# Optimization experiments

Hardware: AMD Instinct MI355X
Metric: run time of the kernel (lower is better)

The kernel has to match this reference:

```python
import jax, jax.numpy as jnp
import numpy as np

BS, NPTS, NQ, N, E = 8, 4096, 4096, 1024, 8192
F_, D, DY, H, OUT, STEPS = 256, 2, 3, 256, 3, 16


def setup_inputs() -> dict:
    key = jax.random.key(0)
    ks = jax.random.split(key, 12)
    s = 0.05
    return {
        "inp_x": jax.random.uniform(ks[0], (BS, NPTS, D), dtype=jnp.float32),
        "inp_y": jax.random.normal(ks[1], (BS, NPTS, DY), dtype=jnp.float32),
        "q": jax.random.uniform(ks[2], (BS, NQ, D), dtype=jnp.float32),
        "node_pos": jax.random.uniform(ks[3], (N, D), dtype=jnp.float32),
        "W_e1": jax.random.normal(ks[4], (D + DY, H), dtype=jnp.float32) * s,
        "b_e1": jnp.zeros((H,), jnp.float32),
        "W_e2": jax.random.normal(ks[5], (H, F_), dtype=jnp.float32) * s,
        "b_e2": jnp.zeros((F_,), jnp.float32),
        "W_g": jax.random.normal(ks[6], (F_ + D, F_), dtype=jnp.float32) * s,
        "b_g": jnp.zeros((F_,), jnp.float32),
        "ln_g": jnp.ones((F_,), jnp.float32),
        "ln_b": jnp.zeros((F_,), jnp.float32),
        "W_d1": jax.random.normal(ks[7], (F_ + D, H), dtype=jnp.float32) * s,
        "b_d1": jnp.zeros((H,), jnp.float32),
        "W_d2": jax.random.normal(ks[8], (H, OUT), dtype=jnp.float32) * s,
        "b_d2": jnp.zeros((OUT,), jnp.float32),
        "edge_index": jax.random.randint(ks[9], (2, E), 0, N, dtype=jnp.int32),
        "msg_steps": STEPS,
    }


def _mlp(x, W1, b1, W2, b2):
    # 2-layer ReLU MLP (matches repo's NN encoder/decoder structure)
    return jnp.maximum(x @ W1 + b1, 0.0) @ W2 + b2


def _soft_coord(pos, x):
    # GENSoftNN repr_fn: softmax over nodes of -||x - pos||^2.
    # pos [N,D], x [B,P,D] -> [B,P,N]; expand ||x-p||^2 to avoid [B,P,N,D].
    d = (jnp.sum(x * x, -1)[..., None]
         + jnp.sum(pos * pos, -1)[None, None, :]
         - 2.0 * jnp.einsum('bpd,nd->bpn', x, pos))
    return jax.nn.softmax(-d, axis=-1)


def _layer_norm(x, g, b, eps=1e-5):
    m = jnp.mean(x, -1, keepdims=True)
    v = jnp.mean((x - m) ** 2, -1, keepdims=True)  # biased var, torch LN
    return (x - m) * jax.lax.rsqrt(v + eps) * g + b


def reference(inp_x, inp_y, q, node_pos, W_e1, b_e1, W_e2, b_e2, W_g, b_g,
              ln_g, ln_b, W_d1, b_d1, W_d2, b_d2, edge_index, msg_steps):
    n = node_pos.shape[0]
    # --- GCNConv symmetric normalization with self-loops (PyG default) ---
    loops = jnp.arange(n, dtype=edge_index.dtype)
    src = jnp.concatenate([edge_index[0], loops])  # message source (x_j)
    dst = jnp.concatenate([edge_index[1], loops])  # aggregation target
    deg = jnp.zeros((n,), jnp.float32).at[dst].add(1.0)
    dinv = jax.lax.rsqrt(jnp.maximum(deg, 1e-12))
    norm = (dinv[src] * dinv[dst])[None, :, None]  # [1, E+N, 1]

    # --- encode input points and project onto nodes ---
    enc = _mlp(jnp.concatenate([inp_x, inp_y], -1), W_e1, b_e1, W_e2, b_e2)  # [B,P,F]
    inp_coord = _soft_coord(node_pos, inp_x)                                  # [B,P,N]
    x = jnp.einsum('bpn,bpf->bnf', inp_coord, enc)                            # [B,N,F]

    pos_b = jnp.broadcast_to(node_pos[None], (x.shape[0], n, node_pos.shape[1]))

    # --- msg_steps of  LN(x + GCNConv(cat(pos, x))) ---
    def step(x, _):
        h = jnp.concatenate([pos_b, x], -1) @ W_g        # lin first: [B,N,F]
        msg = h[:, src, :] * norm                         # gather + scale
        agg = jnp.zeros_like(h).at[:, dst, :].add(msg) + b_g  # scatter-add
        return _layer_norm(x + agg, ln_g, ln_b), None

    x, _ = jax.lax.scan(step, x, None, length=msg_steps)

    # --- decode queries ---
    q_coord = _soft_coord(node_pos, q)                    # [B,Q,N]
    lat = jnp.einsum('bqn,bnf->bqf', q_coord, x)          # [B,Q,F]
    return _mlp(jnp.concatenate([lat, q], -1), W_d1, b_d1, W_d2, b_d2)
```

## Files before the change

kernel.cpp:

```cpp
#include <hip/hip_runtime.h>

#define BB 8
#define NP 4096
#define NN 1024
#define NE 8192
#define FF 256
#define TS 264
#define NSTEP 16
#define NSEG 64
#define SEGSZ 128

typedef float f32x4_t __attribute__((ext_vector_type(4)));
typedef __bf16 bf16x8_t __attribute__((ext_vector_type(8)));
typedef unsigned int u32x4_t __attribute__((ext_vector_type(4)));
typedef unsigned int u32x2_t __attribute__((ext_vector_type(2)));

static __device__ __forceinline__ unsigned short f2bf(float f) {
  return __builtin_bit_cast(unsigned short, static_cast<__bf16>(f));
}
static __device__ __forceinline__ float ashf(unsigned short s) {
  union { unsigned u; float f; } t; t.u = (unsigned)s << 16; return t.f;
}
static __device__ __forceinline__ void split_pk(float a, float b, unsigned& h, unsigned& l) {
  unsigned short ha = f2bf(a), hb = f2bf(b);
  unsigned short la = f2bf(a - ashf(ha)), lb = f2bf(b - ashf(hb));
  h = (unsigned)ha | ((unsigned)hb << 16);
  l = (unsigned)la | ((unsigned)lb << 16);
}
static __device__ __forceinline__ f32x4_t mfma16(u32x4_t a, u32x4_t b, f32x4_t c) {
  return __builtin_amdgcn_mfma_f32_16x16x32_bf16(
      __builtin_bit_cast(bf16x8_t, a), __builtin_bit_cast(bf16x8_t, b), c, 0, 0, 0);
}
static __device__ __forceinline__ int swz16(int e) { return e ^ ((e >> 3) & 7); }

__global__ __launch_bounds__(1024) void k_cnt(const int* __restrict__ dstA,
                                              int* __restrict__ cntg) {
  __shared__ int ds[SEGSZ];
  int seg = blockIdx.x, n = threadIdx.x;
  if (n < SEGSZ) ds[n] = dstA[seg * SEGSZ + n];
  __syncthreads();
  int c = 0;
  #pragma unroll 8
  for (int e = 0; e < SEGSZ; e++) c += (ds[e] == n) ? 1 : 0;
  cntg[seg * NN + n] = c;
}

__global__ __launch_bounds__(1024) void k_scan2(const int* __restrict__ cntg,
    float* __restrict__ dinv, int* __restrict__ csr_off) {
  __shared__ int s[NN];
  int n = threadIdx.x;
  int c = 1;
  for (int sg = 0; sg < NSEG; sg++) c += cntg[sg * NN + n];
  dinv[n] = rsqrtf((float)c);
  s[n] = c;
  __syncthreads();
  for (int st = 1; st < NN; st <<= 1) {
    int v = (n >= st) ? s[n - st] : 0;
    __syncthreads();
    s[n] += v;
    __syncthreads();
  }
  csr_off[n] = s[n] - c;
  if (n == NN - 1) csr_off[NN] = s[n];
}

__global__ __launch_bounds__(1024) void k_fill2(const int* __restrict__ srcA,
    const int* __restrict__ dstA, const float* __restrict__ dinv,
    const int* __restrict__ csr_off, const int* __restrict__ cntg,
    int* __restrict__ csr_src, float* __restrict__ csr_w) {
  int n = threadIdx.x;
  if (blockIdx.x == NSEG) {
    int pos = csr_off[n + 1] - 1;
    csr_src[pos] = n;
    csr_w[pos] = dinv[n] * dinv[n];
    return;
  }
  __shared__ int ds[SEGSZ], ss[SEGSZ];
  int seg = blockIdx.x;
  if (n < SEGSZ) { ds[n] = dstA[seg * SEGSZ + n]; ss[n] = srcA[seg * SEGSZ + n]; }
  __syncthreads();
  int base = csr_off[n];
  for (int s2 = 0; s2 < seg; s2++) base += cntg[s2 * NN + n];
  float dn = dinv[n];
  for (int e = 0; e < SEGSZ; e++) {
    if (ds[e] == n) {
      int sv = ss[e];
      csr_src[base] = sv;
      csr_w[base] = dinv[sv] * dn;
      base++;
    }
  }
}

__global__ __launch_bounds__(256) void k_spos(const float* __restrict__ npos,
    const int* __restrict__ csr_off, const int* __restrict__ csr_src,
    const float* __restrict__ csr_w, float* __restrict__ spos) {
  int n = blockIdx.x * 256 + threadIdx.x;
  if (n >= NN) return;
  float sx = 0.f, sy = 0.f;
  int e1 = csr_off[n + 1];
  for (int e = csr_off[n]; e < e1; e++) {
    float w = csr_w[e]; int s = csr_src[e];
    sx += w * npos[2 * s]; sy += w * npos[2 * s + 1];
  }
  spos[2 * n] = sx; spos[2 * n + 1] = sy;
}

__global__ __launch_bounds__(256) void k_posb(const float* __restrict__ spos,
    const float* __restrict__ Wg, const float* __restrict__ bg, float* __restrict__ sposW) {
  int n = blockIdx.x, f = threadIdx.x;
  sposW[(size_t)n * FF + f] = spos[2 * n] * Wg[f] + spos[2 * n + 1] * Wg[FF + f] + bg[f];
}

__global__ __launch_bounds__(256) void k_stats(const float* __restrict__ inx,
    const float* __restrict__ qxy, const float* __restrict__ npos,
    float* __restrict__ mI, float* __restrict__ liI,
    float* __restrict__ mQ, float* __restrict__ liQ) {
  const float* xy = blockIdx.y ? qxy : inx;
  float* mOut = blockIdx.y ? mQ : mI;
  float* liOut = blockIdx.y ? liQ : liI;
  int wv = threadIdx.x >> 6, lane = threadIdx.x & 63;
  int pt = blockIdx.x * 4 + wv;
  float px = xy[pt * 2], py = xy[pt * 2 + 1];
  float s[16];
  float m = -1e30f;
  #pragma unroll
  for (int k = 0; k < 16; k++) {
    int n = lane + 64 * k;
    float2 np = ((const float2*)npos)[n];
    float dx = px - np.x, dy = py - np.y;
    float v = -(dx * dx + dy * dy);
    s[k] = v; m = fmaxf(m, v);
  }
  #pragma unroll
  for (int o = 32; o; o >>= 1) m = fmaxf(m, __shfl_xor(m, o));
  float l = 0.f;
  #pragma unroll
  for (int k = 0; k < 16; k++) l += __expf(s[k] - m);
  #pragma unroll
  for (int o = 32; o; o >>= 1) l += __shfl_xor(l, o);
  if (lane == 0) { mOut[pt] = m; liOut[pt] = 1.0f / l; }
}

__global__ __launch_bounds__(256) void k_pack_w(const float* __restrict__ We2,
    const float* __restrict__ Wg, const float* __restrict__ Wd1,
    unsigned short* __restrict__ WTe2h, unsigned short* __restrict__ WTe2l,
    unsigned short* __restrict__ WTgh, unsigned short* __restrict__ WTgl,
    unsigned short* __restrict__ WTd1h, unsigned short* __restrict__ WTd1l) {
  int kc = blockIdx.x, which = blockIdx.y, n = threadIdx.x;
  const float* W = (which == 0) ? We2 : (which == 1) ? (Wg + 2 * FF) : Wd1;
  unsigned short* Dh = (which == 0) ? WTe2h : (which == 1) ? WTgh : WTd1h;
  unsigned short* Dl = (which == 0) ? WTe2l : (which == 1) ? WTgl : WTd1l;
  unsigned hu[16], lu[16];
  #pragma unroll
  for (int i = 0; i < 16; i++) {
    float a = W[(kc * 32 + 2 * i) * FF + n];
    float b = W[(kc * 32 + 2 * i + 1) * FF + n];
    split_pk(a, b, hu[i], lu[i]);
  }
  u32x4_t* dvh = (u32x4_t*)(Dh + ((size_t)kc * 256 + n) * 32);
  u32x4_t* dvl = (u32x4_t*)(Dl + ((size_t)kc * 256 + n) * 32);
  #pragma unroll
  for (int i = 0; i < 4; i++) {
    u32x4_t th = {hu[4 * i], hu[4 * i + 1], hu[4 * i + 2], hu[4 * i + 3]};
    u32x4_t tl = {lu[4 * i], lu[4 * i + 1], lu[4 * i + 2], lu[4 * i + 3]};
    dvh[i] = th; dvl[i] = tl;
  }
}

__global__ __launch_bounds__(256) void k_encoder(const float* __restrict__ inx,
    const float* __restrict__ iny, const float* __restrict__ We1,
    const float* __restrict__ be1, const unsigned short* __restrict__ WTe2h,
    const unsigned short* __restrict__ WTe2l, const float* __restrict__ be2,
    unsigned short* __restrict__ encTh, unsigned short* __restrict__ encTl) {
  __shared__ float xin[32][8];
  __shared__ float h[32][TS];
  __shared__ unsigned short Bh[8192];
  __shared__ unsigned short Bl[8192];
  int tid = threadIdx.x;
  int row0 = blockIdx.x * 32;
  int wv = tid >> 6, L = tid & 63, lhi = L >> 4, llo = L & 15;

  if (tid < 160) {
    int pt = tid / 5, d = tid % 5;
    int r = row0 + pt;
    xin[pt][d] = (d < 2) ? inx[r * 2 + d] : iny[r * 3 + (d - 2)];
  }
  __syncthreads();
  {
    int f = tid;
    float w0 = We1[f], w1 = We1[256 + f], w2 = We1[512 + f], w3 = We1[768 + f], w4 = We1[1024 + f];
    float bb = be1[f];
    #pragma unroll 4
    for (int pt = 0; pt < 32; pt++) {
      float v = bb + xin[pt][0]*w0 + xin[pt][1]*w1 + xin[pt][2]*w2 + xin[pt][3]*w3 + xin[pt][4]*w4;
      h[pt][f] = fmaxf(v, 0.f);
    }
  }

  f32x4_t acc[2][4];
  #pragma unroll
  for (int cb = 0; cb < 4; cb++) {
    float bc = be2[wv * 64 + cb * 16 + llo];
    f32x4_t t = {bc, bc, bc, bc};
    acc[0][cb] = t; acc[1][cb] = t;
  }

  for (int kc = 0; kc < 8; kc++) {
    __syncthreads();
    {
      const u32x4_t* sh = (const u32x4_t*)(WTe2h + (size_t)kc * 8192);
      const u32x4_t* sl = (const u32x4_t*)(WTe2l + (size_t)kc * 8192);
      u32x4_t* dh = (u32x4_t*)Bh;
      u32x4_t* dl = (u32x4_t*)Bl;
      #pragma unroll
      for (int i = 0; i < 4; i++) {
        int e = tid + i * 256;
        int es = swz16(e);
        dh[es] = sh[e]; dl[es] = sl[e];
      }
    }
    __syncthreads();
    int kbase = kc * 32 + lhi * 8;
    u32x4_t a0h, a0l, a1h, a1l;
    {
      float p[8];
      *(f32x4_t*)p = *(const f32x4_t*)&h[llo][kbase];
      *(f32x4_t*)(p + 4) = *(const f32x4_t*)&h[llo][kbase + 4];
      unsigned hw[4], lw[4];
      #pragma unroll
      for (int i = 0; i < 4; i++) split_pk(p[2 * i], p[2 * i + 1], hw[i], lw[i]);
      u32x4_t th = {hw[0], hw[1], hw[2], hw[3]}; a0h = th;
      u32x4_t tl = {lw[0], lw[1], lw[2], lw[3]}; a0l = tl;
    }
    {
      float p[8];
      *(f32x4_t*)p = *(const f32x4_t*)&h[llo + 16][kbase];
      *(f32x4_t*)(p + 4) = *(const f32x4_t*)&h[llo + 16][kbase + 4];
      unsigned hw[4], lw[4];
      #pragma unroll
      for (int i = 0; i < 4; i++) split_pk(p[2 * i], p[2 * i + 1], hw[i], lw[i]);
      u32x4_t th = {hw[0], hw[1], hw[2], hw[3]}; a1h = th;
      u32x4_t tl = {lw[0], lw[1], lw[2], lw[3]}; a1l = tl;
    }
    #pragma unroll
    for (int cb = 0; cb < 4; cb++) {
      int col = wv * 64 + cb * 16 + llo;
      int off = swz16(col * 4 + lhi) * 8;
      u32x4_t bh = *(const u32x4_t*)&Bh[off];
      u32x4_t bl = *(const u32x4_t*)&Bl[off];
      acc[0][cb] = mfma16(a0h, bh, mfma16(a0h, bl, mfma16(a0l, bh, acc[0][cb])));
      acc[1][cb] = mfma16(a1h, bh, mfma16(a1h, bl, mfma16(a1l, bh, acc[1][cb])));
    }
  }
  #pragma unroll
  for (int rb = 0; rb < 2; rb++)
    #pragma unroll
    for (int cb = 0; cb < 4; cb++) {
      int col = wv * 64 + cb * 16 + llo;
      f32x4_t v = acc[rb][cb];
      size_t idx = ((size_t)blockIdx.x * 256 + col) * 32 + rb * 16 + lhi * 4;
      unsigned hw0, lw0, hw1, lw1;
      split_pk(v[0], v[1], hw0, lw0);
      split_pk(v[2], v[3], hw1, lw1);
      u32x2_t wh = {hw0, hw1}; *(u32x2_t*)&encTh[idx] = wh;
      u32x2_t wl = {lw0, lw1}; *(u32x2_t*)&encTl[idx] = wl;
    }
}

__global__ __launch_bounds__(256, 4) void k_proj1(const float* __restrict__ inx,
    const float* __restrict__ mI, const float* __restrict__ liI,
    const float* __restrict__ npos, const unsigned short* __restrict__ encTh,
    const unsigned short* __restrict__ encTl, float* __restrict__ part) {
  __shared__ unsigned short BstH[8192];
  __shared__ unsigned short BstL[8192];
  __shared__ unsigned short AstH[1024];
  __shared__ unsigned short AstL[1024];
  int tid = threadIdx.x;
  int id = blockIdx.x;
  int xcd = id & 7, kid = id >> 3;
  int slice = xcd * 4 + (kid >> 5);
  int n0 = (kid & 31) * 32;
  int b = slice >> 2, z = slice & 3;
  int wv = tid >> 6, L = tid & 63, lhi = L >> 4, llo = L & 15;
  int an = tid >> 3, t7 = tid & 7, ap = t7 * 4;
  float2 npv = ((const float2*)npos)[n0 + an];
  int pbase0 = b * NP + z * 1024;
  int aoff = swz16(an * 4 + (t7 >> 1)) * 8 + (t7 & 1) * 4;

  u32x4_t rbh[4], rbl[4];
  unsigned ch0, ch1, cl0, cl1;

  auto coordA = [&](int kc) {
    int p = pbase0 + kc * 32 + ap;
    float c[4];
    #pragma unroll
    for (int j = 0; j < 4; j++) {
      float2 pxy = ((const float2*)inx)[p + j];
      float mm = mI[p + j], ll = liI[p + j];
      float dx = pxy.x - npv.x, dy = pxy.y - npv.y;
      c[j] = __expf(-(dx * dx + dy * dy) - mm) * ll;
    }
    split_pk(c[0], c[1], ch0, cl0);
    split_pk(c[2], c[3], ch1, cl1);
  };
  auto loadB = [&](int kc) {
    const u32x4_t* sh = (const u32x4_t*)(encTh + (size_t)(b * 128 + z * 32 + kc) * 8192);
    const u32x4_t* sl = (const u32x4_t*)(encTl + (size_t)(b * 128 + z * 32 + kc) * 8192);
    #pragma unroll
    for (int i = 0; i < 4; i++) { rbh[i] = sh[tid + i * 256]; rbl[i] = sl[tid + i * 256]; }
  };

  f32x4_t acc[2][4];
  #pragma unroll
  for (int i = 0; i < 2; i++)
    #pragma unroll
    for (int j = 0; j < 4; j++) { f32x4_t t = {0.f, 0.f, 0.f, 0.f}; acc[i][j] = t; }

  coordA(0);
  loadB(0);
  int a0off = swz16(llo * 4 + lhi) * 8;
  int a1off = swz16((llo + 16) * 4 + lhi) * 8;
  for (int kc = 0; kc < 32; kc++) {
    __syncthreads();
    #pragma unroll
    for (int i = 0; i < 4; i++) {
      int es = swz16(tid + i * 256);
      ((u32x4_t*)BstH)[es] = rbh[i];
      ((u32x4_t*)BstL)[es] = rbl[i];
    }
    { u32x2_t wh = {ch0, ch1}; *(u32x2_t*)&AstH[aoff] = wh; }
    { u32x2_t wl = {cl0, cl1}; *(u32x2_t*)&AstL[aoff] = wl; }
    __syncthreads();
    if (kc < 31) { loadB(kc + 1); coordA(kc + 1); }
    u32x4_t a0h = *(const u32x4_t*)&AstH[a0off];
    u32x4_t a0l = *(const u32x4_t*)&AstL[a0off];
    u32x4_t a1h = *(const u32x4_t*)&AstH[a1off];
    u32x4_t a1l = *(const u32x4_t*)&AstL[a1off];
    #pragma unroll
    for (int cb = 0; cb < 4; cb++) {
      int off = swz16((wv * 64 + cb * 16 + llo) * 4 + lhi) * 8;
      u32x4_t bh = *(const u32x4_t*)&BstH[off];
      u32x4_t bl = *(const u32x4_t*)&BstL[off];
      acc[0][cb] = mfma16(a0h, bh, mfma16(a0h, bl, mfma16(a0l, bh, acc[0][cb])));
      acc[1][cb] = mfma16(a1h, bh, mfma16(a1h, bl, mfma16(a1l, bh, acc[1][cb])));
    }
  }
  float* op = part + (((size_t)(z * BB + b)) * NN + n0) * FF;
  #pragma unroll
  for (int rb = 0; rb < 2; rb++)
    #pragma unroll
    for (int cb = 0; cb < 4; cb++) {
      int col = wv * 64 + cb * 16 + llo;
      f32x4_t v = acc[rb][cb];
      #pragma unroll
      for (int r = 0; r < 4; r++) op[(rb * 16 + lhi * 4 + r) * FF + col] = v[r];
    }
}

__global__ __launch_bounds__(256) void k_reduce(const float* __restrict__ part,
                                                float* __restrict__ x) {
  size_t i = ((size_t)blockIdx.x * 256 + threadIdx.x) * 4;
  const size_t S = (size_t)BB * NN * FF;
  f32x4_t a = *(const f32x4_t*)&part[i];
  f32x4_t b = *(const f32x4_t*)&part[S + i];
  f32x4_t c = *(const f32x4_t*)&part[2 * S + i];
  f32x4_t d = *(const f32x4_t*)&part[3 * S + i];
  f32x4_t r = (a + b) + (c + d);
  *(f32x4_t*)&x[i] = r;
}

__global__ __launch_bounds__(512) void k_msg2(const float* __restrict__ x_in,
    float* __restrict__ x_out, const float* __restrict__ sposW,
    const int* __restrict__ coff, const int* __restrict__ csrc,
    const float* __restrict__ csw, const unsigned short* __restrict__ WTgh,
    const unsigned short* __restrict__ WTgl, const float* __restrict__ lng,
    const float* __restrict__ lnb, int last,
    unsigned short* __restrict__ xTh, unsigned short* __restrict__ xTl) {
  __shared__ unsigned Ah[32][132];
  __shared__ unsigned Al[32][132];
  __shared__ unsigned short Bh[2][8192];
  __shared__ unsigned short Bl[2][8192];
  __shared__ float redS[32][8];
  __shared__ float redQ[32][8];
  int tid = threadIdx.x;
  int id = blockIdx.x;
  int b = id & 7;
  int nb = id >> 3;
  int n0 = nb * 32;
  int wv = tid >> 6, L = tid & 63, lhi = L >> 4, llo = L & 15;

  u32x4_t rbh[2], rbl[2];
  auto loadB = [&](int kc) {
    const u32x4_t* sh = (const u32x4_t*)(WTgh + (size_t)kc * 8192);
    const u32x4_t* sl = (const u32x4_t*)(WTgl + (size_t)kc * 8192);
    #pragma unroll
    for (int i = 0; i < 2; i++) { rbh[i] = sh[tid + i * 512]; rbl[i] = sl[tid + i * 512]; }
  };
  auto writeB = [&](int buf) {
    u32x4_t* dh = (u32x4_t*)Bh[buf];
    u32x4_t* dl = (u32x4_t*)Bl[buf];
    #pragma unroll
    for (int i = 0; i < 2; i++) {
      int es = swz16(tid + i * 512);
      dh[es] = rbh[i]; dl[es] = rbl[i];
    }
  };

  loadB(0);

  {
    int row = tid >> 4, seg = tid & 15;
    int n = n0 + row;
    float g[16];
    #pragma unroll
    for (int i = 0; i < 16; i++) g[i] = 0.f;
    int e0 = coff[n], e1 = coff[n + 1];
    for (int e = e0; e < e1; e++) {
      float w = csw[e];
      int s = csrc[e];
      const f32x4_t* px = (const f32x4_t*)(x_in + ((size_t)b * NN + s) * FF + seg * 16);
      #pragma unroll
      for (int i = 0; i < 4; i++) {
        f32x4_t v = px[i];
        g[4*i]   += w * v[0]; g[4*i+1] += w * v[1];
        g[4*i+2] += w * v[2]; g[4*i+3] += w * v[3];
      }
    }
    #pragma unroll
    for (int i = 0; i < 8; i++) {
      unsigned h, l;
      split_pk(g[2 * i], g[2 * i + 1], h, l);
      Ah[row][seg * 8 + i] = h;
      Al[row][seg * 8 + i] = l;
    }
  }
  writeB(0);
  __syncthreads();

  f32x4_t acc[2][2];
  #pragma unroll
  for (int i = 0; i < 2; i++)
    #pragma unroll
    for (int j = 0; j < 2; j++) { f32x4_t t = {0.f, 0.f, 0.f, 0.f}; acc[i][j] = t; }

  for (int kc = 0; kc < 8; kc++) {
    int cur = kc & 1;
    if (kc < 7) loadB(kc + 1);
    u32x4_t a0h = *(const u32x4_t*)&Ah[llo][kc * 16 + lhi * 4];
    u32x4_t a0l = *(const u32x4_t*)&Al[llo][kc * 16 + lhi * 4];
    u32x4_t a1h = *(const u32x4_t*)&Ah[llo + 16][kc * 16 + lhi * 4];
    u32x4_t a1l = *(const u32x4_t*)&Al[llo + 16][kc * 16 + lhi * 4];
    #pragma unroll
    for (int cb = 0; cb < 2; cb++) {
      int off = swz16((wv * 32 + cb * 16 + llo) * 4 + lhi) * 8;
      u32x4_t bh = *(const u32x4_t*)&Bh[cur][off];
      u32x4_t bl = *(const u32x4_t*)&Bl[cur][off];
      acc[0][cb] = mfma16(a0h, bh, mfma16(a0h, bl, mfma16(a0l, bh, acc[0][cb])));
      acc[1][cb] = mfma16(a1h, bh, mfma16(a1h, bl, mfma16(a1l, bh, acc[1][cb])));
    }
    if (kc < 7) writeB(cur ^ 1);
    __syncthreads();
  }

  #pragma unroll
  for (int rb = 0; rb < 2; rb++)
    #pragma unroll
    for (int cb = 0; cb < 2; cb++) {
      int col = wv * 32 + cb * 16 + llo;
      #pragma unroll
      for (int r = 0; r < 4; r++) {
        int row = rb * 16 + lhi * 4 + r;
        float sw = sposW[(size_t)(n0 + row) * FF + col];
        float xr = x_in[((size_t)b * NN + n0 + row) * FF + col];
        acc[rb][cb][r] += sw + xr;
      }
    }
  float ps[2][4], pq[2][4];
  #pragma unroll
  for (int rb = 0; rb < 2; rb++)
    #pragma unroll
    for (int r = 0; r < 4; r++) {
      float s = 0.f, q = 0.f;
      #pragma unroll
      for (int cb = 0; cb < 2; cb++) { float y = acc[rb][cb][r]; s += y; q += y * y; }
      #pragma unroll
      for (int m = 1; m < 16; m <<= 1) { s += __shfl_xor(s, m); q += __shfl_xor(q, m); }
      ps[rb][r] = s; pq[rb][r] = q;
    }
  if (llo == 0) {
    #pragma unroll
    for (int rb = 0; rb < 2; rb++)
      #pragma unroll
      for (int r = 0; r < 4; r++) {
        int row = rb * 16 + lhi * 4 + r;
        redS[row][wv] = ps[rb][r];
        redQ[row][wv] = pq[rb][r];
      }
  }
  __syncthreads();
  float mrs[2][4][2];
  #pragma unroll
  for (int rb = 0; rb < 2; rb++)
    #pragma unroll
    for (int r = 0; r < 4; r++) {
      int row = rb * 16 + lhi * 4 + r;
      float S = 0.f, Q = 0.f;
      #pragma unroll
      for (int wq = 0; wq < 8; wq++) { S += redS[row][wq]; Q += redQ[row][wq]; }
      float mean = S * (1.f / 256.f);
      float var = Q * (1.f / 256.f) - mean * mean;
      mrs[rb][r][0] = mean;
      mrs[rb][r][1] = rsqrtf(var + 1e-5f);
    }
  #pragma unroll
  for (int cb = 0; cb < 2; cb++) {
    int col = wv * 32 + cb * 16 + llo;
    float gg = lng[col], bb = lnb[col];
    #pragma unroll
    for (int rb = 0; rb < 2; rb++)
      #pragma unroll
      for (int r = 0; r < 4; r++) {
        int row = rb * 16 + lhi * 4 + r;
        float o = (acc[rb][cb][r] - mrs[rb][r][0]) * mrs[rb][r][1] * gg + bb;
        if (!last) {
          x_out[((size_t)b * NN + n0 + row) * FF + col] = o;
        } else {
          size_t idx = (((size_t)b * 32 + nb) * 256 + col) * 32 + row;
          unsigned short hh = f2bf(o);
          xTh[idx] = hh;
          xTl[idx] = f2bf(o - ashf(hh));
        }
      }
  }
}

__global__ __launch_bounds__(256, 3) void k_proj2(const float* __restrict__ qxy,
    const float* __restrict__ mQ, const float* __restrict__ liQ,
    const float* __restrict__ npos, const unsigned short* __restrict__ xTh,
    const unsigned short* __restrict__ xTl, unsigned short* __restrict__ latTh,
    unsigned short* __restrict__ latTl) {
  __shared__ unsigned short BstH[8192];
  __shared__ unsigned short BstL[8192];
  __shared__ unsigned short AstH[1024];
  __shared__ unsigned short AstL[1024];
  __shared__ float nps[NN * 2];
  int tid = threadIdx.x;
  int id = blockIdx.x;
  int b = id & 7;
  int q0b = id >> 3;
  int q0 = q0b * 32;
  int bt = b * 128 + q0b;
  int wv = tid >> 6, L = tid & 63, lhi = L >> 4, llo = L & 15;
  int aq = tid >> 3, t7 = tid & 7, an4 = t7 * 4;
  int aoff = swz16(aq * 4 + (t7 >> 1)) * 8 + (t7 & 1) * 4;

  {
    const f32x4_t* s4 = (const f32x4_t*)npos;
    *(f32x4_t*)&nps[tid * 4] = s4[tid];
    *(f32x4_t*)&nps[(tid + 256) * 4] = s4[tid + 256];
  }
  int qg = b * NP + q0 + aq;
  float2 qv = ((const float2*)qxy)[qg];
  float qm = mQ[qg], qli = liQ[qg];
  __syncthreads();

  u32x4_t rbh[4], rbl[4];
  unsigned ch0, ch1, cl0, cl1;

  auto coordA = [&](int kc) {
    int nb = kc * 32 + an4;
    float c[4];
    #pragma unroll
    for (int j = 0; j < 4; j++) {
      float nx = nps[(nb + j) * 2], ny = nps[(nb + j) * 2 + 1];
      float dx = qv.x - nx, dy = qv.y - ny;
      c[j] = __expf(-(dx * dx + dy * dy) - qm) * qli;
    }
    split_pk(c[0], c[1], ch0, cl0);
    split_pk(c[2], c[3], ch1, cl1);
  };
  auto loadB = [&](int kc) {
    const u32x4_t* sh = (const u32x4_t*)(xTh + (size_t)(b * 32 + kc) * 8192);
    const u32x4_t* sl = (const u32x4_t*)(xTl + (size_t)(b * 32 + kc) * 8192);
    #pragma unroll
    for (int i = 0; i < 4; i++) { rbh[i] = sh[tid + i * 256]; rbl[i] = sl[tid + i * 256]; }
  };

  f32x4_t acc[2][4];
  #pragma unroll
  for (int i = 0; i < 2; i++)
    #pragma unroll
    for (int j = 0; j < 4; j++) { f32x4_t t = {0.f, 0.f, 0.f, 0.f}; acc[i][j] = t; }

  coordA(0);
  loadB(0);
  int a0off = swz16(llo * 4 + lhi) * 8;
  int a1off = swz16((llo + 16) * 4 + lhi) * 8;
  for (int kc = 0; kc < 32; kc++) {
    __syncthreads();
    #pragma unroll
    for (int i = 0; i < 4; i++) {
      int es = swz16(tid + i * 256);
      ((u32x4_t*)BstH)[es] = rbh[i];
      ((u32x4_t*)BstL)[es] = rbl[i];
    }
    { u32x2_t wh = {ch0, ch1}; *(u32x2_t*)&AstH[aoff] = wh; }
    { u32x2_t wl = {cl0, cl1}; *(u32x2_t*)&AstL[aoff] = wl; }
    __syncthreads();
    if (kc < 31) { loadB(kc + 1); coordA(kc + 1); }
    u32x4_t a0h = *(const u32x4_t*)&AstH[a0off];
    u32x4_t a0l = *(const u32x4_t*)&AstL[a0off];
    u32x4_t a1h = *(const u32x4_t*)&AstH[a1off];
    u32x4_t a1l = *(const u32x4_t*)&AstL[a1off];
    #pragma unroll
    for (int cb = 0; cb < 4; cb++) {
      int off = swz16((wv * 64 + cb * 16 + llo) * 4 + lhi) * 8;
      u32x4_t bh = *(const u32x4_t*)&BstH[off];
      u32x4_t bl = *(const u32x4_t*)&BstL[off];
      acc[0][cb] = mfma16(a0h, bh, mfma16(a0h, bl, mfma16(a0l, bh, acc[0][cb])));
      acc[1][cb] = mfma16(a1h, bh, mfma16(a1h, bl, mfma16(a1l, bh, acc[1][cb])));
    }
  }
  #pragma unroll
  for (int rb = 0; rb < 2; rb++)
    #pragma unroll
    for (int cb = 0; cb < 4; cb++) {
      int col = wv * 64 + cb * 16 + llo;
      int fc = col >> 5, kk = col & 31;
      f32x4_t v = acc[rb][cb];
      #pragma unroll
      for (int r = 0; r < 4; r++) {
        size_t idx = ((size_t)bt * 8 + fc) * 1024 + (rb * 16 + lhi * 4 + r) * 32 + kk;
        unsigned short hh = f2bf(v[r]);
        latTh[idx] = hh;
        latTl[idx] = f2bf(v[r] - ashf(hh));
      }
    }
}

__global__ __launch_bounds__(256, 4) void k_decoder(const unsigned short* __restrict__ latTh,
    const unsigned short* __restrict__ latTl, const float* __restrict__ qxy,
    const unsigned short* __restrict__ WTd1h, const unsigned short* __restrict__ WTd1l,
    const float* __restrict__ bd1, const float* __restrict__ Wd1,
    const float* __restrict__ Wd2, const float* __restrict__ bd2, float* __restrict__ out) {
  __shared__ unsigned short BstH[8192];
  __shared__ unsigned short BstL[8192];
  __shared__ unsigned short AstH[1024];
  __shared__ unsigned short AstL[1024];
  __shared__ float qs[32][2];
  __shared__ float red[4][32][3];
  int tid = threadIdx.x;
  int bt = blockIdx.x;
  int wv = tid >> 6, L = tid & 63, lhi = L >> 4, llo = L & 15;

  u32x4_t rbh[4], rbl[4], ra;
  auto loadB = [&](int kc) {
    const u32x4_t* sh = (const u32x4_t*)(WTd1h + (size_t)kc * 8192);
    const u32x4_t* sl = (const u32x4_t*)(WTd1l + (size_t)kc * 8192);
    #pragma unroll
    for (int i = 0; i < 4; i++) { rbh[i] = sh[tid + i * 256]; rbl[i] = sl[tid + i * 256]; }
  };
  auto loadA = [&](int kc) {
    if (tid < 128)
      ra = ((const u32x4_t*)(latTh + ((size_t)bt * 8 + kc) * 1024))[tid];
    else
      ra = ((const u32x4_t*)(latTl + ((size_t)bt * 8 + kc) * 1024))[tid - 128];
  };

  if (tid < 64) qs[tid >> 1][tid & 1] = qxy[((size_t)bt * 32 + (tid >> 1)) * 2 + (tid & 1)];
  loadB(0); loadA(0);
  __syncthreads();

  f32x4_t acc[2][4];
  #pragma unroll
  for (int cb = 0; cb < 4; cb++) {
    int col = wv * 64 + cb * 16 + llo;
    float wa = Wd1[256 * FF + col], wb = Wd1[257 * FF + col], bc = bd1[col];
    #pragma unroll
    for (int rb = 0; rb < 2; rb++) {
      f32x4_t t;
      #pragma unroll
      for (int r = 0; r < 4; r++) {
        int row = rb * 16 + lhi * 4 + r;
        t[r] = bc + qs[row][0] * wa + qs[row][1] * wb;
      }
      acc[rb][cb] = t;
    }
  }

  int a0off = swz16(llo * 4 + lhi) * 8;
  int a1off = swz16((llo + 16) * 4 + lhi) * 8;
  for (int kc = 0; kc < 8; kc++) {
    __syncthreads();
    #pragma unroll
    for (int i = 0; i < 4; i++) {
      int es = swz16(tid + i * 256);
      ((u32x4_t*)BstH)[es] = rbh[i];
      ((u32x4_t*)BstL)[es] = rbl[i];
    }
    if (tid < 128) ((u32x4_t*)AstH)[swz16(tid)] = ra;
    else ((u32x4_t*)AstL)[swz16(tid - 128)] = ra;
    __syncthreads();
    if (kc < 7) { loadB(kc + 1); loadA(kc + 1); }
    u32x4_t a0h = *(const u32x4_t*)&AstH[a0off];
    u32x4_t a0l = *(const u32x4_t*)&AstL[a0off];
    u32x4_t a1h = *(const u32x4_t*)&AstH[a1off];
    u32x4_t a1l = *(const u32x4_t*)&AstL[a1off];
    #pragma unroll
    for (int cb = 0; cb < 4; cb++) {
      int off = swz16((wv * 64 + cb * 16 + llo) * 4 + lhi) * 8;
      u32x4_t bh = *(const u32x4_t*)&BstH[off];
      u32x4_t bl = *(const u32x4_t*)&BstL[off];
      acc[0][cb] = mfma16(a0h, bh, mfma16(a0h, bl, mfma16(a0l, bh, acc[0][cb])));
      acc[1][cb] = mfma16(a1h, bh, mfma16(a1h, bl, mfma16(a1l, bh, acc[1][cb])));
    }
  }

  float po[2][4][3];
  #pragma unroll
  for (int rb = 0; rb < 2; rb++)
    #pragma unroll
    for (int r = 0; r < 4; r++) { po[rb][r][0] = 0.f; po[rb][r][1] = 0.f; po[rb][r][2] = 0.f; }
  #pragma unroll
  for (int rb = 0; rb < 2; rb++)
    #pragma unroll
    for (int cb = 0; cb < 4; cb++) {
      int col = wv * 64 + cb * 16 + llo;
      float w0 = Wd2[col * 3], w1 = Wd2[col * 3 + 1], w2 = Wd2[col * 3 + 2];
      f32x4_t v = acc[rb][cb];
      #pragma unroll
      for (int r = 0; r < 4; r++) {
        float hv = fmaxf(v[r], 0.f);
        po[rb][r][0] += hv * w0; po[rb][r][1] += hv * w1; po[rb][r][2] += hv * w2;
      }
    }
  #pragma unroll
  for (int o = 8; o; o >>= 1)
    #pragma unroll
    for (int rb = 0; rb < 2; rb++)
      #pragma unroll
      for (int r = 0; r < 4; r++) {
        po[rb][r][0] += __shfl_xor(po[rb][r][0], o);
        po[rb][r][1] += __shfl_xor(po[rb][r][1], o);
        po[rb][r][2] += __shfl_xor(po[rb][r][2], o);
      }
  if (llo == 0) {
    #pragma unroll
    for (int rb = 0; rb < 2; rb++)
      #pragma unroll
      for (int r = 0; r < 4; r++) {
        int row = rb * 16 + lhi * 4 + r;
        red[wv][row][0] = po[rb][r][0];
        red[wv][row][1] = po[rb][r][1];
        red[wv][row][2] = po[rb][r][2];
      }
  }
  __syncthreads();
  if (tid < 96) {
    int row = tid / 3, o = tid % 3;
    float s = red[0][row][o] + red[1][row][o] + red[2][row][o] + red[3][row][o] + bd2[o];
    out[((size_t)bt * 32 + row) * 3 + o] = s;
  }
}

extern "C" void kernel_launch(void* const* d_in, const int* in_sizes, int n_in,
                              void* d_out, int out_size, void* d_ws, size_t ws_size,
                              hipStream_t stream) {
  const float* inx = (const float*)d_in[0];
  const float* iny = (const float*)d_in[1];
  const float* qxy = (const float*)d_in[2];
  const float* npos = (const float*)d_in[3];
  const float* We1 = (const float*)d_in[4];
  const float* be1 = (const float*)d_in[5];
  const float* We2 = (const float*)d_in[6];
  const float* be2 = (const float*)d_in[7];
  const float* Wg  = (const float*)d_in[8];
  const float* bg  = (const float*)d_in[9];
  const float* lng = (const float*)d_in[10];
  const float* lnb = (const float*)d_in[11];
  const float* Wd1 = (const float*)d_in[12];
  const float* bd1 = (const float*)d_in[13];
  const float* Wd2 = (const float*)d_in[14];
  const float* bd2 = (const float*)d_in[15];
  const int* eidx  = (const int*)d_in[16];
  float* out = (float*)d_out;

  char* w = (char*)d_ws;
  auto carve = [&](size_t n) { char* p = w; w += (n + 255) & ~(size_t)255; return p; };
  char* encR = carve((size_t)2 * BB * NP * FF * 2);
  unsigned short* encTh = (unsigned short*)encR;
  unsigned short* encTl = (unsigned short*)(encR + (size_t)BB * NP * FF * 2);
  unsigned short* latTh = encTh;
  unsigned short* latTl = encTl;
  float* xA = (float*)carve((size_t)BB * NN * FF * 4);
  float* xB = (float*)carve((size_t)BB * NN * FF * 4);
  unsigned short* xTh = (unsigned short*)carve((size_t)BB * NN * FF * 2);
  unsigned short* xTl = (unsigned short*)carve((size_t)BB * NN * FF * 2);
  float* part = (float*)carve((size_t)4 * BB * NN * FF * 4);
  float* mI   = (float*)carve((size_t)BB * NP * 4);
  float* liI  = (float*)carve((size_t)BB * NP * 4);
  float* mQ   = (float*)carve((size_t)BB * NP * 4);
  float* liQ  = (float*)carve((size_t)BB * NP * 4);
  unsigned short* WTe2h = (unsigned short*)carve((size_t)8 * 256 * 32 * 2);
  unsigned short* WTe2l = (unsigned short*)carve((size_t)8 * 256 * 32 * 2);
  unsigned short* WTgh  = (unsigned short*)carve((size_t)8 * 256 * 32 * 2);
  unsigned short* WTgl  = (unsigned short*)carve((size_t)8 * 256 * 32 * 2);
  unsigned short* WTd1h = (unsigned short*)carve((size_t)8 * 256 * 32 * 2);
  unsigned short* WTd1l = (unsigned short*)carve((size_t)8 * 256 * 32 * 2);
  float* sposW = (float*)carve((size_t)NN * FF * 4);
  float* dinv = (float*)carve(NN * 4);
  float* spos = (float*)carve(NN * 2 * 4);
  float* csw  = (float*)carve((NE + NN) * 4);
  int* coff   = (int*)carve((NN + 1) * 4);
  int* csrc   = (int*)carve((NE + NN) * 4);
  int* cntg   = (int*)carve((size_t)NSEG * NN * 4);

  const int* esrc = eidx;
  const int* edst = eidx + NE;

  k_cnt<<<dim3(NSEG), dim3(1024), 0, stream>>>(edst, cntg);
  k_scan2<<<dim3(1), dim3(1024), 0, stream>>>(cntg, dinv, coff);
  k_fill2<<<dim3(NSEG + 1), dim3(1024), 0, stream>>>(esrc, edst, dinv, coff, cntg, csrc, csw);
  k_spos<<<dim3(4), dim3(256), 0, stream>>>(npos, coff, csrc, csw, spos);
  k_posb<<<dim3(NN), dim3(256), 0, stream>>>(spos, Wg, bg, sposW);
  k_pack_w<<<dim3(8, 3), dim3(256), 0, stream>>>(We2, Wg, Wd1, WTe2h, WTe2l, WTgh, WTgl,
                                                 WTd1h, WTd1l);

  k_stats<<<dim3(BB * NP / 4, 2), dim3(256), 0, stream>>>(inx, qxy, npos, mI, liI, mQ, liQ);
  k_encoder<<<dim3(BB * NP / 32), dim3(256), 0, stream>>>(inx, iny, We1, be1, WTe2h, WTe2l, be2,
                                                          encTh, encTl);
  k_proj1<<<dim3(1024), dim3(256), 0, stream>>>(inx, mI, liI, npos, encTh, encTl, part);
  k_reduce<<<dim3(BB * NN * FF / 1024), dim3(256), 0, stream>>>(part, xA);
  for (int s = 0; s < NSTEP; s++) {
    const float* xi = (s & 1) ? xB : xA;
    float* xo = (s & 1) ? xA : xB;
    k_msg2<<<dim3(256), dim3(512), 0, stream>>>(xi, xo, sposW, coff, csrc, csw,
                                                WTgh, WTgl, lng, lnb,
                                                (s == NSTEP - 1) ? 1 : 0, xTh, xTl);
  }
  k_proj2<<<dim3(1024), dim3(256), 0, stream>>>(qxy, mQ, liQ, npos, xTh, xTl, latTh, latTl);
  k_decoder<<<dim3(BB * NP / 32), dim3(256), 0, stream>>>(latTh, latTl, qxy, WTd1h, WTd1l,
                                                          bd1, Wd1, Wd2, bd2, out);
}
```

Measured before the change: 561.2 us.

## Double M-tile in projection GEMMs to 64 rows and prefetch residual in msg

k_proj1 and k_proj2 now compute 64-row output tiles instead of 32 per block. Each B tile loaded into shared memory is reused across four row-blocks, and the grid is halved. This cuts global traffic for encT/xT and the shared-memory staging per MFMA, at the cost of more accumulator registers and a lower launch-bounds occupancy hint. Separately, k_msg2 loads the sposW + x residual before the MFMA loop so that global latency overlaps with the compute.

```diff
diff --git a/kernel.cpp b/kernel.cpp
--- a/kernel.cpp
+++ b/kernel.cpp
@@ -268,41 +268,43 @@
     }
 }
 
-__global__ __launch_bounds__(256, 4) void k_proj1(const float* __restrict__ inx,
+__global__ __launch_bounds__(256, 3) void k_proj1(const float* __restrict__ inx,
     const float* __restrict__ mI, const float* __restrict__ liI,
     const float* __restrict__ npos, const unsigned short* __restrict__ encTh,
     const unsigned short* __restrict__ encTl, float* __restrict__ part) {
   __shared__ unsigned short BstH[8192];
   __shared__ unsigned short BstL[8192];
-  __shared__ unsigned short AstH[1024];
-  __shared__ unsigned short AstL[1024];
+  __shared__ unsigned short AstH[2048];
+  __shared__ unsigned short AstL[2048];
   int tid = threadIdx.x;
   int id = blockIdx.x;
   int xcd = id & 7, kid = id >> 3;
-  int slice = xcd * 4 + (kid >> 5);
-  int n0 = (kid & 31) * 32;
+  int slice = xcd * 4 + (kid >> 4);
+  int n0 = (kid & 15) * 64;
   int b = slice >> 2, z = slice & 3;
   int wv = tid >> 6, L = tid & 63, lhi = L >> 4, llo = L & 15;
-  int an = tid >> 3, t7 = tid & 7, ap = t7 * 4;
+  int an = tid >> 2, t3 = tid & 3, ap = t3 * 8;
   float2 npv = ((const float2*)npos)[n0 + an];
   int pbase0 = b * NP + z * 1024;
-  int aoff = swz16(an * 4 + (t7 >> 1)) * 8 + (t7 & 1) * 4;
-
-  u32x4_t rbh[4], rbl[4];
-  unsigned ch0, ch1, cl0, cl1;
+  int aoff = swz16(an * 4 + t3) * 8;
+
+  u32x4_t rbh[4], rbl[4], chv, clv;
 
   auto coordA = [&](int kc) {
     int p = pbase0 + kc * 32 + ap;
-    float c[4];
-    #pragma unroll
-    for (int j = 0; j < 4; j++) {
+    float c[8];
+    #pragma unroll
+    for (int j = 0; j < 8; j++) {
       float2 pxy = ((const float2*)inx)[p + j];
       float mm = mI[p + j], ll = liI[p + j];
       float dx = pxy.x - npv.x, dy = pxy.y - npv.y;
       c[j] = __expf(-(dx * dx + dy * dy) - mm) * ll;
     }
-    split_pk(c[0], c[1], ch0, cl0);
-    split_pk(c[2], c[3], ch1, cl1);
+    unsigned h[4], l[4];
+    #pragma unroll
+    for (int j = 0; j < 4; j++) split_pk(c[2 * j], c[2 * j + 1], h[j], l[j]);
+    u32x4_t th = {h[0], h[1], h[2], h[3]}; chv = th;
+    u32x4_t tl = {l[0], l[1], l[2], l[3]}; clv = tl;
   };
   auto loadB = [&](int kc) {
     const u32x4_t* sh = (const u32x4_t*)(encTh + (size_t)(b * 128 + z * 32 + kc) * 8192);
@@ -311,16 +313,17 @@
     for (int i = 0; i < 4; i++) { rbh[i] = sh[tid + i * 256]; rbl[i] = sl[tid + i * 256]; }
   };
 
-  f32x4_t acc[2][4];
-  #pragma unroll
-  for (int i = 0; i < 2; i++)
+  f32x4_t acc[4][4];
+  #pragma unroll
+  for (int i = 0; i < 4; i++)
     #pragma unroll
     for (int j = 0; j < 4; j++) { f32x4_t t = {0.f, 0.f, 0.f, 0.f}; acc[i][j] = t; }
 
   coordA(0);
   loadB(0);
-  int a0off = swz16(llo * 4 + lhi) * 8;
-  int a1off = swz16((llo + 16) * 4 + lhi) * 8;
+  int aroff[4];
+  #pragma unroll
+  for (int rb = 0; rb < 4; rb++) aroff[rb] = swz16((llo + 16 * rb) * 4 + lhi) * 8;
   for (int kc = 0; kc < 32; kc++) {
     __syncthreads();
     #pragma unroll
@@ -329,26 +332,29 @@
       ((u32x4_t*)BstH)[es] = rbh[i];
       ((u32x4_t*)BstL)[es] = rbl[i];
     }
-    { u32x2_t wh = {ch0, ch1}; *(u32x2_t*)&AstH[aoff] = wh; }
-    { u32x2_t wl = {cl0, cl1}; *(u32x2_t*)&AstL[aoff] = wl; }
+    *(u32x4_t*)&AstH[aoff] = chv;
+    *(u32x4_t*)&AstL[aoff] = clv;
     __syncthreads();
     if (kc < 31) { loadB(kc + 1); coordA(kc + 1); }
-    u32x4_t a0h = *(const u32x4_t*)&AstH[a0off];
-    u32x4_t a0l = *(const u32x4_t*)&AstL[a0off];
-    u32x4_t a1h = *(const u32x4_t*)&AstH[a1off];
-    u32x4_t a1l = *(const u32x4_t*)&AstL[a1off];
+    u32x4_t ah[4], al[4];
+    #pragma unroll
+    for (int rb = 0; rb < 4; rb++) {
+      ah[rb] = *(const u32x4_t*)&AstH[aroff[rb]];
+      al[rb] = *(const u32x4_t*)&AstL[aroff[rb]];
+    }
     #pragma unroll
     for (int cb = 0; cb < 4; cb++) {
       int off = swz16((wv * 64 + cb * 16 + llo) * 4 + lhi) * 8;
       u32x4_t bh = *(const u32x4_t*)&BstH[off];
       u32x4_t bl = *(const u32x4_t*)&BstL[off];
-      acc[0][cb] = mfma16(a0h, bh, mfma16(a0h, bl, mfma16(a0l, bh, acc[0][cb])));
-      acc[1][cb] = mfma16(a1h, bh, mfma16(a1h, bl, mfma16(a1l, bh, acc[1][cb])));
+      #pragma unroll
+      for (int rb = 0; rb < 4; rb++)
+        acc[rb][cb] = mfma16(ah[rb], bh, mfma16(ah[rb], bl, mfma16(al[rb], bh, acc[rb][cb])));
     }
   }
   float* op = part + (((size_t)(z * BB + b)) * NN + n0) * FF;
   #pragma unroll
-  for (int rb = 0; rb < 2; rb++)
+  for (int rb = 0; rb < 4; rb++)
     #pragma unroll
     for (int cb = 0; cb < 4; cb++) {
       int col = wv * 64 + cb * 16 + llo;
@@ -436,6 +442,20 @@
     }
   }
   writeB(0);
+
+  f32x4_t szr[2][2];
+  #pragma unroll
+  for (int rb = 0; rb < 2; rb++)
+    #pragma unroll
+    for (int cb = 0; cb < 2; cb++) {
+      int col = wv * 32 + cb * 16 + llo;
+      #pragma unroll
+      for (int r = 0; r < 4; r++) {
+        int row = rb * 16 + lhi * 4 + r;
+        szr[rb][cb][r] = sposW[(size_t)(n0 + row) * FF + col]
+                       + x_in[((size_t)b * NN + n0 + row) * FF + col];
+      }
+    }
   __syncthreads();
 
   f32x4_t acc[2][2];
@@ -467,14 +487,8 @@
   for (int rb = 0; rb < 2; rb++)
     #pragma unroll
     for (int cb = 0; cb < 2; cb++) {
-      int col = wv * 32 + cb * 16 + llo;
-      #pragma unroll
-      for (int r = 0; r < 4; r++) {
-        int row = rb * 16 + lhi * 4 + r;
-        float sw = sposW[(size_t)(n0 + row) * FF + col];
-        float xr = x_in[((size_t)b * NN + n0 + row) * FF + col];
-        acc[rb][cb][r] += sw + xr;
-      }
+      #pragma unroll
+      for (int r = 0; r < 4; r++) acc[rb][cb][r] += szr[rb][cb][r];
     }
   float ps[2][4], pq[2][4];
   #pragma unroll
@@ -542,18 +556,17 @@
     unsigned short* __restrict__ latTl) {
   __shared__ unsigned short BstH[8192];
   __shared__ unsigned short BstL[8192];
-  __shared__ unsigned short AstH[1024];
-  __shared__ unsigned short AstL[1024];
+  __shared__ unsigned short AstH[2048];
+  __shared__ unsigned short AstL[2048];
   __shared__ float nps[NN * 2];
   int tid = threadIdx.x;
   int id = blockIdx.x;
   int b = id & 7;
-  int q0b = id >> 3;
-  int q0 = q0b * 32;
-  int bt = b * 128 + q0b;
+  int q64 = id >> 3;
+  int q0 = q64 * 64;
   int wv = tid >> 6, L = tid & 63, lhi = L >> 4, llo = L & 15;
-  int aq = tid >> 3, t7 = tid & 7, an4 = t7 * 4;
-  int aoff = swz16(aq * 4 + (t7 >> 1)) * 8 + (t7 & 1) * 4;
+  int aq = tid >> 2, t3 = tid & 3, an8 = t3 * 8;
+  int aoff = swz16(aq * 4 + t3) * 8;
 
   {
     const f32x4_t* s4 = (const f32x4_t*)npos;
@@ -565,20 +578,22 @@
   float qm = mQ[qg], qli = liQ[qg];
   __syncthreads();
 
-  u32x4_t rbh[4], rbl[4];
-  unsigned ch0, ch1, cl0, cl1;
+  u32x4_t rbh[4], rbl[4], chv, clv;
 
   auto coordA = [&](int kc) {
-    int nb = kc * 32 + an4;
-    float c[4];
-    #pragma unroll
-    for (int j = 0; j < 4; j++) {
+    int nb = kc * 32 + an8;
+    float c[8];
+    #pragma unroll
+    for (int j = 0; j < 8; j++) {
       float nx = nps[(nb + j) * 2], ny = nps[(nb + j) * 2 + 1];
       float dx = qv.x - nx, dy = qv.y - ny;
       c[j] = __expf(-(dx * dx + dy * dy) - qm) * qli;
     }
-    split_pk(c[0], c[1], ch0, cl0);
-    split_pk(c[2], c[3], ch1, cl1);
+    unsigned h[4], l[4];
+    #pragma unroll
+    for (int j = 0; j < 4; j++) split_pk(c[2 * j], c[2 * j + 1], h[j], l[j]);
+    u32x4_t th = {h[0], h[1], h[2], h[3]}; chv = th;
+    u32x4_t tl = {l[0], l[1], l[2], l[3]}; clv = tl;
   };
   auto loadB = [&](int kc) {
     const u32x4_t* sh = (const u32x4_t*)(xTh + (size_t)(b * 32 + kc) * 8192);
@@ -587,16 +602,17 @@
     for (int i = 0; i < 4; i++) { rbh[i] = sh[tid + i * 256]; rbl[i] = sl[tid + i * 256]; }
   };
 
-  f32x4_t acc[2][4];
-  #pragma unroll
-  for (int i = 0; i < 2; i++)
+  f32x4_t acc[4][4];
+  #pragma unroll
+  for (int i = 0; i < 4; i++)
     #pragma unroll
     for (int j = 0; j < 4; j++) { f32x4_t t = {0.f, 0.f, 0.f, 0.f}; acc[i][j] = t; }
 
   coordA(0);
   loadB(0);
-  int a0off = swz16(llo * 4 + lhi) * 8;
-  int a1off = swz16((llo + 16) * 4 + lhi) * 8;
+  int aroff[4];
+  #pragma unroll
+  for (int rb = 0; rb < 4; rb++) aroff[rb] = swz16((llo + 16 * rb) * 4 + lhi) * 8;
   for (int kc = 0; kc < 32; kc++) {
     __syncthreads();
     #pragma unroll
@@ -605,25 +621,28 @@
       ((u32x4_t*)BstH)[es] = rbh[i];
       ((u32x4_t*)BstL)[es] = rbl[i];
     }
-    { u32x2_t wh = {ch0, ch1}; *(u32x2_t*)&AstH[aoff] = wh; }
-    { u32x2_t wl = {cl0, cl1}; *(u32x2_t*)&AstL[aoff] = wl; }
+    *(u32x4_t*)&AstH[aoff] = chv;
+    *(u32x4_t*)&AstL[aoff] = clv;
     __syncthreads();
     if (kc < 31) { loadB(kc + 1); coordA(kc + 1); }
-    u32x4_t a0h = *(const u32x4_t*)&AstH[a0off];
-    u32x4_t a0l = *(const u32x4_t*)&AstL[a0off];
-    u32x4_t a1h = *(const u32x4_t*)&AstH[a1off];
-    u32x4_t a1l = *(const u32x4_t*)&AstL[a1off];
+    u32x4_t ah[4], al[4];
+    #pragma unroll
+    for (int rb = 0; rb < 4; rb++) {
+      ah[rb] = *(const u32x4_t*)&AstH[aroff[rb]];
+      al[rb] = *(const u32x4_t*)&AstL[aroff[rb]];
+    }
     #pragma unroll
     for (int cb = 0; cb < 4; cb++) {
       int off = swz16((wv * 64 + cb * 16 + llo) * 4 + lhi) * 8;
       u32x4_t bh = *(const u32x4_t*)&BstH[off];
       u32x4_t bl = *(const u32x4_t*)&BstL[off];
-      acc[0][cb] = mfma16(a0h, bh, mfma16(a0h, bl, mfma16(a0l, bh, acc[0][cb])));
-      acc[1][cb] = mfma16(a1h, bh, mfma16(a1h, bl, mfma16(a1l, bh, acc[1][cb])));
-    }
-  }
-  #pragma unroll
-  for (int rb = 0; rb < 2; rb++)
+      #pragma unroll
+      for (int rb = 0; rb < 4; rb++)
+        acc[rb][cb] = mfma16(ah[rb], bh, mfma16(ah[rb], bl, mfma16(al[rb], bh, acc[rb][cb])));
+    }
+  }
+  #pragma unroll
+  for (int rb = 0; rb < 4; rb++)
     #pragma unroll
     for (int cb = 0; cb < 4; cb++) {
       int col = wv * 64 + cb * 16 + llo;
@@ -631,7 +650,9 @@
       f32x4_t v = acc[rb][cb];
       #pragma unroll
       for (int r = 0; r < 4; r++) {
-        size_t idx = ((size_t)bt * 8 + fc) * 1024 + (rb * 16 + lhi * 4 + r) * 32 + kk;
+        int row = rb * 16 + lhi * 4 + r;
+        int bt = b * 128 + q64 * 2 + (row >> 5);
+        size_t idx = ((size_t)bt * 8 + fc) * 1024 + (row & 31) * 32 + kk;
         unsigned short hh = f2bf(v[r]);
         latTh[idx] = hh;
         latTl[idx] = f2bf(v[r] - ashf(hh));
@@ -830,7 +851,7 @@
   k_stats<<<dim3(BB * NP / 4, 2), dim3(256), 0, stream>>>(inx, qxy, npos, mI, liI, mQ, liQ);
   k_encoder<<<dim3(BB * NP / 32), dim3(256), 0, stream>>>(inx, iny, We1, be1, WTe2h, WTe2l, be2,
                                                           encTh, encTl);
-  k_proj1<<<dim3(1024), dim3(256), 0, stream>>>(inx, mI, liI, npos, encTh, encTl, part);
+  k_proj1<<<dim3(512), dim3(256), 0, stream>>>(inx, mI, liI, npos, encTh, encTl, part);
   k_reduce<<<dim3(BB * NN * FF / 1024), dim3(256), 0, stream>>>(part, xA);
   for (int s = 0; s < NSTEP; s++) {
     const float* xi = (s & 1) ? xB : xA;
@@ -839,7 +860,7 @@
                                                 WTgh, WTgl, lng, lnb,
                                                 (s == NSTEP - 1) ? 1 : 0, xTh, xTl);
   }
-  k_proj2<<<dim3(1024), dim3(256), 0, stream>>>(qxy, mQ, liQ, npos, xTh, xTl, latTh, latTl);
+  k_proj2<<<dim3(512), dim3(256), 0, stream>>>(qxy, mQ, liQ, npos, xTh, xTl, latTh, latTl);
   k_decoder<<<dim3(BB * NP / 32), dim3(256), 0, stream>>>(latTh, latTl, qxy, WTd1h, WTd1l,
                                                           bd1, Wd1, Wd2, bd2, out);
 }
```

Result: faster. 547.7 us (-2.4%).
